# Kernel optimization log

Measured on AMD Instinct MI355X. Metric: run time of the kernel, lower is better.

## Reference

```python
import jax, jax.numpy as jnp
import numpy as np

D = 512
H = 8
HD = D // H
EPS = 1e-5
NEG_INF = -1e30


def _ln(x, g, b):
    mu = jnp.mean(x, axis=-1, keepdims=True)
    var = jnp.mean(jnp.square(x - mu), axis=-1, keepdims=True)
    return (x - mu) * jax.lax.rsqrt(var + EPS) * g + b


def setup_inputs() -> dict:
    key = jax.random.key(0)
    ks = jax.random.split(key, 8)
    V, M, S = 128, 128, 514  # seq includes 2 head tokens (cls+dist)
    inp = {
        "video_embeds": jax.random.normal(ks[0], (V, D), jnp.float32),
        "music_features": jax.random.normal(ks[1], (M, S, D), jnp.float32),
        "music_masks": jnp.ones((M, S - 2), jnp.int32),
    }
    wk = jax.random.split(ks[2], 5)
    for name, k in zip(["Wq", "Wk", "Wv", "Wo", "Wl"], wk):
        inp[name] = jax.random.normal(k, (D, D), jnp.float32) * 0.02
    for name in ["bq", "bk", "bv", "bo", "bl"]:
        inp[name] = jnp.zeros((D,), jnp.float32)
    for name in ["g1", "g2", "g3"]:
        inp[name] = jnp.ones((D,), jnp.float32)
    for name in ["b1", "b2", "b3"]:
        inp[name] = jnp.zeros((D,), jnp.float32)
    return inp


def reference(video_embeds, music_features, music_masks,
              Wq, bq, Wk, bk, Wv, bv, Wo, bo, Wl, bl,
              g1, b1, g2, b2, g3, b3):
    # drop cls + dist tokens
    mf = music_features[:, 2:, :]  # (M, f, D)
    ve = _ln(video_embeds, g1, b1)  # (V, D)
    mf = _ln(mf, g1, b1)
    V = ve.shape[0]
    M, f, _ = mf.shape

    q = (ve @ Wq.T + bq).reshape(V, H, HD).transpose(1, 0, 2)        # (H, V, hd)
    k = (mf @ Wk.T + bk).reshape(M, f, H, HD).transpose(0, 2, 1, 3)  # (M, H, f, hd)
    v = (mf @ Wv.T + bv).reshape(M, f, H, HD).transpose(0, 2, 1, 3)  # (M, H, f, hd)

    logits = jnp.einsum('hvd,mhfd->vmhf', q, k) / np.sqrt(HD).astype(np.float32)
    mask = music_masks[None, :, None, :]  # (1, M, 1, f)
    logits = jnp.where(mask == 0, NEG_INF, logits)
    w = jax.nn.softmax(logits, axis=-1)
    attn = jnp.einsum('vmhf,mhfd->vmhd', w, v).reshape(V, M, D)
    attn = attn @ Wo.T + bo

    attn = _ln(attn, g2, b2)
    out = attn + (attn @ Wl.T + bl)  # dropout = identity in eval
    return _ln(out, g3, b3)
```

## Files before the change

### kernel.cpp

```cpp
#include <hip/hip_runtime.h>
#include <hip/hip_bf16.h>

typedef unsigned int uint;
typedef unsigned short ushort;
typedef __bf16 bf16;
typedef bf16 bf16x8 __attribute__((ext_vector_type(8)));
typedef float f32x4 __attribute__((ext_vector_type(4)));
typedef ushort ushort4v __attribute__((ext_vector_type(4)));

__device__ __forceinline__ float bf2f(ushort u) {
  union { uint u; float f; } v; v.u = ((uint)u) << 16; return v.f;
}
__device__ __forceinline__ ushort f2bf(float f) {
  union { float f; uint u; } v; v.f = f;
  uint u = v.u;
  uint r = (u + 0x7fffu + ((u >> 16) & 1u)) >> 16;
  return (ushort)r;
}

__device__ __forceinline__ void gl2lds16(const void* g, void* l) {
  __builtin_amdgcn_global_load_lds(
      (const __attribute__((address_space(1))) void*)g,
      (__attribute__((address_space(3))) void*)l, 16, 0, 0);
}

__device__ __forceinline__ void ln_rows0(
    int nrows, int blk, int nblk, int tid,
    const float* __restrict__ srcA,
    const float* __restrict__ g, const float* __restrict__ b,
    ushort* __restrict__ dst)
{
  const int l = tid & 63;
  const int nw = nblk * 4;
  for (int row = blk * 4 + (tid >> 6); row < nrows; row += nw) {
    const float* s = srcA + (size_t)row * 512;
    float x[8];
    float4 a0 = *(const float4*)(s + l * 4);
    float4 a1 = *(const float4*)(s + 256 + l * 4);
    x[0] = a0.x; x[1] = a0.y; x[2] = a0.z; x[3] = a0.w;
    x[4] = a1.x; x[5] = a1.y; x[6] = a1.z; x[7] = a1.w;
    float sum = 0.f, sq = 0.f;
    #pragma unroll
    for (int j = 0; j < 8; ++j) { sum += x[j]; sq += x[j] * x[j]; }
    #pragma unroll
    for (int o = 1; o < 64; o <<= 1) {
      sum += __shfl_xor(sum, o);
      sq  += __shfl_xor(sq, o);
    }
    float mu = sum * (1.f / 512.f);
    float var = sq * (1.f / 512.f) - mu * mu;
    float rstd = rsqrtf(var + 1e-5f);
    float4 g0 = *(const float4*)(g + l * 4);
    float4 g1 = *(const float4*)(g + 256 + l * 4);
    float4 b0 = *(const float4*)(b + l * 4);
    float4 b1 = *(const float4*)(b + 256 + l * 4);
    float gv[8] = {g0.x,g0.y,g0.z,g0.w,g1.x,g1.y,g1.z,g1.w};
    float bv[8] = {b0.x,b0.y,b0.z,b0.w,b1.x,b1.y,b1.z,b1.w};
    ushort* d = dst + (size_t)row * 512;
    ushort4v p0, p1;
    #pragma unroll
    for (int j = 0; j < 4; ++j) {
      p0[j] = f2bf((x[j] - mu) * rstd * gv[j] + bv[j]);
      p1[j] = f2bf((x[4+j] - mu) * rstd * gv[4+j] + bv[4+j]);
    }
    *(ushort4v*)(d + l * 4) = p0;
    *(ushort4v*)(d + 256 + l * 4) = p1;
  }
}

__device__ __forceinline__ void ln_pair(
    int mode, int wid, int tid,
    const void* __restrict__ srcA, const void* __restrict__ srcB,
    const float* __restrict__ g, const float* __restrict__ b,
    void* __restrict__ dst)
{
  const int l = tid & 63;
  const int r0 = wid * 2, r1 = r0 + 1;
  float x0[8], x1[8];
  if (mode == 1) {
    int mm0 = r0 >> 9, fi0 = r0 & 511;
    int mm1 = r1 >> 9, fi1 = r1 & 511;
    const float* s0 = (const float*)srcA + ((size_t)mm0 * 514 + 2 + fi0) * 512;
    const float* s1 = (const float*)srcA + ((size_t)mm1 * 514 + 2 + fi1) * 512;
    float4 a0 = *(const float4*)(s0 + l * 4);
    float4 a1 = *(const float4*)(s0 + 256 + l * 4);
    float4 c0 = *(const float4*)(s1 + l * 4);
    float4 c1 = *(const float4*)(s1 + 256 + l * 4);
    x0[0]=a0.x; x0[1]=a0.y; x0[2]=a0.z; x0[3]=a0.w;
    x0[4]=a1.x; x0[5]=a1.y; x0[6]=a1.z; x0[7]=a1.w;
    x1[0]=c0.x; x1[1]=c0.y; x1[2]=c0.z; x1[3]=c0.w;
    x1[4]=c1.x; x1[5]=c1.y; x1[6]=c1.z; x1[7]=c1.w;
  } else if (mode == 2) {
    const ushort* s0 = (const ushort*)srcA + (size_t)r0 * 512;
    const ushort* s1 = (const ushort*)srcA + (size_t)r1 * 512;
    uint4 u0 = *(const uint4*)(s0 + l * 8);
    uint4 u1 = *(const uint4*)(s1 + l * 8);
    x0[0]=bf2f((ushort)u0.x); x0[1]=bf2f((ushort)(u0.x>>16));
    x0[2]=bf2f((ushort)u0.y); x0[3]=bf2f((ushort)(u0.y>>16));
    x0[4]=bf2f((ushort)u0.z); x0[5]=bf2f((ushort)(u0.z>>16));
    x0[6]=bf2f((ushort)u0.w); x0[7]=bf2f((ushort)(u0.w>>16));
    x1[0]=bf2f((ushort)u1.x); x1[1]=bf2f((ushort)(u1.x>>16));
    x1[2]=bf2f((ushort)u1.y); x1[3]=bf2f((ushort)(u1.y>>16));
    x1[4]=bf2f((ushort)u1.z); x1[5]=bf2f((ushort)(u1.z>>16));
    x1[6]=bf2f((ushort)u1.w); x1[7]=bf2f((ushort)(u1.w>>16));
  } else {
    const ushort* sa0 = (const ushort*)srcA + (size_t)r0 * 512;
    const ushort* sb0 = (const ushort*)srcB + (size_t)r0 * 512;
    const ushort* sa1 = (const ushort*)srcA + (size_t)r1 * 512;
    const ushort* sb1 = (const ushort*)srcB + (size_t)r1 * 512;
    uint4 ua0 = *(const uint4*)(sa0 + l * 8);
    uint4 ub0 = *(const uint4*)(sb0 + l * 8);
    uint4 ua1 = *(const uint4*)(sa1 + l * 8);
    uint4 ub1 = *(const uint4*)(sb1 + l * 8);
    x0[0]=bf2f((ushort)ua0.x)+bf2f((ushort)ub0.x);
    x0[1]=bf2f((ushort)(ua0.x>>16))+bf2f((ushort)(ub0.x>>16));
    x0[2]=bf2f((ushort)ua0.y)+bf2f((ushort)ub0.y);
    x0[3]=bf2f((ushort)(ua0.y>>16))+bf2f((ushort)(ub0.y>>16));
    x0[4]=bf2f((ushort)ua0.z)+bf2f((ushort)ub0.z);
    x0[5]=bf2f((ushort)(ua0.z>>16))+bf2f((ushort)(ub0.z>>16));
    x0[6]=bf2f((ushort)ua0.w)+bf2f((ushort)ub0.w);
    x0[7]=bf2f((ushort)(ua0.w>>16))+bf2f((ushort)(ub0.w>>16));
    x1[0]=bf2f((ushort)ua1.x)+bf2f((ushort)ub1.x);
    x1[1]=bf2f((ushort)(ua1.x>>16))+bf2f((ushort)(ub1.x>>16));
    x1[2]=bf2f((ushort)ua1.y)+bf2f((ushort)ub1.y);
    x1[3]=bf2f((ushort)(ua1.y>>16))+bf2f((ushort)(ub1.y>>16));
    x1[4]=bf2f((ushort)ua1.z)+bf2f((ushort)ub1.z);
    x1[5]=bf2f((ushort)(ua1.z>>16))+bf2f((ushort)(ub1.z>>16));
    x1[6]=bf2f((ushort)ua1.w)+bf2f((ushort)ub1.w);
    x1[7]=bf2f((ushort)(ua1.w>>16))+bf2f((ushort)(ub1.w>>16));
  }
  float s0 = 0.f, q0 = 0.f, s1 = 0.f, q1 = 0.f;
  #pragma unroll
  for (int j = 0; j < 8; ++j) {
    s0 += x0[j]; q0 += x0[j] * x0[j];
    s1 += x1[j]; q1 += x1[j] * x1[j];
  }
  #pragma unroll
  for (int o = 1; o < 64; o <<= 1) {
    s0 += __shfl_xor(s0, o); q0 += __shfl_xor(q0, o);
    s1 += __shfl_xor(s1, o); q1 += __shfl_xor(q1, o);
  }
  float mu0 = s0 * (1.f/512.f), mu1 = s1 * (1.f/512.f);
  float rstd0 = rsqrtf(q0 * (1.f/512.f) - mu0 * mu0 + 1e-5f);
  float rstd1 = rsqrtf(q1 * (1.f/512.f) - mu1 * mu1 + 1e-5f);

  float gv[8], bv[8];
  if (mode == 1) {
    float4 g0 = *(const float4*)(g + l * 4);
    float4 g1v = *(const float4*)(g + 256 + l * 4);
    float4 b0 = *(const float4*)(b + l * 4);
    float4 b1v = *(const float4*)(b + 256 + l * 4);
    gv[0]=g0.x; gv[1]=g0.y; gv[2]=g0.z; gv[3]=g0.w;
    gv[4]=g1v.x; gv[5]=g1v.y; gv[6]=g1v.z; gv[7]=g1v.w;
    bv[0]=b0.x; bv[1]=b0.y; bv[2]=b0.z; bv[3]=b0.w;
    bv[4]=b1v.x; bv[5]=b1v.y; bv[6]=b1v.z; bv[7]=b1v.w;
  } else {
    float4 g0 = *(const float4*)(g + l * 8);
    float4 g1v = *(const float4*)(g + l * 8 + 4);
    float4 b0 = *(const float4*)(b + l * 8);
    float4 b1v = *(const float4*)(b + l * 8 + 4);
    gv[0]=g0.x; gv[1]=g0.y; gv[2]=g0.z; gv[3]=g0.w;
    gv[4]=g1v.x; gv[5]=g1v.y; gv[6]=g1v.z; gv[7]=g1v.w;
    bv[0]=b0.x; bv[1]=b0.y; bv[2]=b0.z; bv[3]=b0.w;
    bv[4]=b1v.x; bv[5]=b1v.y; bv[6]=b1v.z; bv[7]=b1v.w;
  }
  if (mode == 1) {
    ushort* d0 = (ushort*)dst + (size_t)r0 * 512;
    ushort* d1 = (ushort*)dst + (size_t)r1 * 512;
    ushort4v p00, p01, p10, p11;
    #pragma unroll
    for (int j = 0; j < 4; ++j) {
      p00[j] = f2bf((x0[j]-mu0)*rstd0*gv[j]+bv[j]);
      p01[j] = f2bf((x0[4+j]-mu0)*rstd0*gv[4+j]+bv[4+j]);
      p10[j] = f2bf((x1[j]-mu1)*rstd1*gv[j]+bv[j]);
      p11[j] = f2bf((x1[4+j]-mu1)*rstd1*gv[4+j]+bv[4+j]);
    }
    *(ushort4v*)(d0 + l * 4) = p00;
    *(ushort4v*)(d0 + 256 + l * 4) = p01;
    *(ushort4v*)(d1 + l * 4) = p10;
    *(ushort4v*)(d1 + 256 + l * 4) = p11;
  } else if (mode == 2) {
    ushort* d0 = (ushort*)dst + (size_t)r0 * 512;
    ushort* d1 = (ushort*)dst + (size_t)r1 * 512;
    uint4 o0, o1;
    float y;
    uint t;
    y = (x0[0]-mu0)*rstd0*gv[0]+bv[0]; t = f2bf(y);
    o0.x = t | ((uint)f2bf((x0[1]-mu0)*rstd0*gv[1]+bv[1]) << 16);
    o0.y = (uint)f2bf((x0[2]-mu0)*rstd0*gv[2]+bv[2]) | ((uint)f2bf((x0[3]-mu0)*rstd0*gv[3]+bv[3]) << 16);
    o0.z = (uint)f2bf((x0[4]-mu0)*rstd0*gv[4]+bv[4]) | ((uint)f2bf((x0[5]-mu0)*rstd0*gv[5]+bv[5]) << 16);
    o0.w = (uint)f2bf((x0[6]-mu0)*rstd0*gv[6]+bv[6]) | ((uint)f2bf((x0[7]-mu0)*rstd0*gv[7]+bv[7]) << 16);
    o1.x = (uint)f2bf((x1[0]-mu1)*rstd1*gv[0]+bv[0]) | ((uint)f2bf((x1[1]-mu1)*rstd1*gv[1]+bv[1]) << 16);
    o1.y = (uint)f2bf((x1[2]-mu1)*rstd1*gv[2]+bv[2]) | ((uint)f2bf((x1[3]-mu1)*rstd1*gv[3]+bv[3]) << 16);
    o1.z = (uint)f2bf((x1[4]-mu1)*rstd1*gv[4]+bv[4]) | ((uint)f2bf((x1[5]-mu1)*rstd1*gv[5]+bv[5]) << 16);
    o1.w = (uint)f2bf((x1[6]-mu1)*rstd1*gv[6]+bv[6]) | ((uint)f2bf((x1[7]-mu1)*rstd1*gv[7]+bv[7]) << 16);
    *(uint4*)(d0 + l * 8) = o0;
    *(uint4*)(d1 + l * 8) = o1;
  } else {
    float* d0 = (float*)dst + (size_t)r0 * 512;
    float* d1 = (float*)dst + (size_t)r1 * 512;
    float4 a0, a1, c0, c1;
    a0.x=(x0[0]-mu0)*rstd0*gv[0]+bv[0]; a0.y=(x0[1]-mu0)*rstd0*gv[1]+bv[1];
    a0.z=(x0[2]-mu0)*rstd0*gv[2]+bv[2]; a0.w=(x0[3]-mu0)*rstd0*gv[3]+bv[3];
    a1.x=(x0[4]-mu0)*rstd0*gv[4]+bv[4]; a1.y=(x0[5]-mu0)*rstd0*gv[5]+bv[5];
    a1.z=(x0[6]-mu0)*rstd0*gv[6]+bv[6]; a1.w=(x0[7]-mu0)*rstd0*gv[7]+bv[7];
    c0.x=(x1[0]-mu1)*rstd1*gv[0]+bv[0]; c0.y=(x1[1]-mu1)*rstd1*gv[1]+bv[1];
    c0.z=(x1[2]-mu1)*rstd1*gv[2]+bv[2]; c0.w=(x1[3]-mu1)*rstd1*gv[3]+bv[3];
    c1.x=(x1[4]-mu1)*rstd1*gv[4]+bv[4]; c1.y=(x1[5]-mu1)*rstd1*gv[5]+bv[5];
    c1.z=(x1[6]-mu1)*rstd1*gv[6]+bv[6]; c1.w=(x1[7]-mu1)*rstd1*gv[7]+bv[7];
    *(float4*)(d0 + l * 8) = a0;
    *(float4*)(d0 + l * 8 + 4) = a1;
    *(float4*)(d1 + l * 8) = c0;
    *(float4*)(d1 + l * 8 + 4) = c1;
  }
}

__global__ __launch_bounds__(256) void ln512p(
    int mode, const void* __restrict__ srcA, const void* __restrict__ srcB,
    const float* __restrict__ g, const float* __restrict__ b,
    void* __restrict__ dst)
{
  ln_pair(mode, blockIdx.x * 4 + (threadIdx.x >> 6), threadIdx.x, srcA, srcB, g, b, dst);
}

struct PreArgs {
  const float* s0; const float* s1; const float* s2; const float* s3; const float* s4;
  ushort* d0; ushort* d1; ushort* d2; ushort* d3; ushort* d4;
  const float* video; const float* music;
  const float* g1; const float* b1;
  ushort* veln; ushort* mfln;
};
__global__ __launch_bounds__(256) void preamble(PreArgs a) {
  int bb = blockIdx.x;
  if (bb < 640) {
    int t = bb * 256 + threadIdx.x;
    int which = t >> 15;
    int e = (t & 32767) * 8;
    const float* s = which == 0 ? a.s0 : which == 1 ? a.s1 : which == 2 ? a.s2 : which == 3 ? a.s3 : a.s4;
    ushort*      d = which == 0 ? a.d0 : which == 1 ? a.d1 : which == 2 ? a.d2 : which == 3 ? a.d3 : a.d4;
    float4 v0 = *(const float4*)(s + e);
    float4 v1 = *(const float4*)(s + e + 4);
    uint4 o;
    o.x = (uint)f2bf(v0.x) | ((uint)f2bf(v0.y) << 16);
    o.y = (uint)f2bf(v0.z) | ((uint)f2bf(v0.w) << 16);
    o.z = (uint)f2bf(v1.x) | ((uint)f2bf(v1.y) << 16);
    o.w = (uint)f2bf(v1.z) | ((uint)f2bf(v1.w) << 16);
    *(uint4*)(d + e) = o;
  } else if (bb < 672) {
    ln_rows0(128, bb - 640, 32, threadIdx.x, a.video, a.g1, a.b1, a.veln);
  } else {
    ln_pair(1, (bb - 672) * 4 + (threadIdx.x >> 6), threadIdx.x,
            a.music, nullptr, a.g1, a.b1, a.mfln);
  }
}

__global__ __launch_bounds__(256) void gemm_t3(
    const ushort* __restrict__ A, const ushort* __restrict__ W,
    const float* __restrict__ bias, ushort* __restrict__ C,
    float scale, int vt_mode,
    const ushort* __restrict__ Aq, const ushort* __restrict__ Wqp,
    const float* __restrict__ bqp, ushort* __restrict__ Qout, int qy)
{
  __shared__ __align__(16) ushort As[2][128 * 64];
  __shared__ __align__(16) ushort Bs[2][128 * 64];
  const int tid = threadIdx.x;
  const int w = tid >> 6, l = tid & 63;
  const int lg = l >> 4, lr = l & 15;
  const int wr = w >> 1, wc = w & 1;

  int row0, col0;
  const bool isq = ((int)blockIdx.y == qy);
  if (isq) {
    A = Aq; W = Wqp; bias = bqp; C = Qout; scale = 0.125f; vt_mode = 0;
    row0 = 0; col0 = blockIdx.x * 128;
  } else {
    int nwg = gridDim.x * (qy >= 0 ? qy : gridDim.y);
    int bid = blockIdx.y * gridDim.x + blockIdx.x;
    if ((nwg & 7) == 0) bid = (bid & 7) * (nwg >> 3) + (bid >> 3);
    row0 = (bid / gridDim.x) * 128;
    col0 = (bid % gridDim.x) * 128;
  }

  f32x4 acc[4][4];
  #pragma unroll
  for (int i = 0; i < 4; i++)
    #pragma unroll
    for (int j = 0; j < 4; j++) { f32x4 z = {0.f,0.f,0.f,0.f}; acc[i][j] = z; }

  size_t asrc[4], wsrc[4]; int ldst[4];
  #pragma unroll
  for (int c2 = 0; c2 < 4; ++c2) {
    int c = c2 * 256 + tid;
    int r = c >> 3, j = c & 7;
    int koff = (j ^ (r & 7)) * 8;
    asrc[c2] = (size_t)(row0 + r) * 512 + koff;
    wsrc[c2] = (size_t)(col0 + r) * 512 + koff;
    ldst[c2] = (c2 * 256 + w * 64) * 8;
  }

  auto stage = [&](int pb, int kk) {
    #pragma unroll
    for (int c2 = 0; c2 < 4; ++c2) {
      gl2lds16(A + asrc[c2] + kk * 64, &As[pb][ldst[c2]]);
      gl2lds16(W + wsrc[c2] + kk * 64, &Bs[pb][ldst[c2]]);
    }
  };
  auto compute = [&](int pb) {
    #pragma unroll
    for (int ks = 0; ks < 2; ++ks) {
      bf16x8 af[4], bfr[4];
      #pragma unroll
      for (int mi = 0; mi < 4; ++mi) {
        int r = wr * 64 + mi * 16 + lr;
        af[mi] = *(const bf16x8*)(&As[pb][r * 64 + ((ks * 32 + lg * 8) ^ ((r & 7) * 8))]);
      }
      #pragma unroll
      for (int ni = 0; ni < 4; ++ni) {
        int r = wc * 64 + ni * 16 + lr;
        bfr[ni] = *(const bf16x8*)(&Bs[pb][r * 64 + ((ks * 32 + lg * 8) ^ ((r & 7) * 8))]);
      }
      #pragma unroll
      for (int mi = 0; mi < 4; ++mi)
        #pragma unroll
        for (int ni = 0; ni < 4; ++ni)
          acc[mi][ni] = __builtin_amdgcn_mfma_f32_16x16x32_bf16(af[mi], bfr[ni], acc[mi][ni], 0, 0, 0);
    }
  };

  stage(0, 0);
  __syncthreads();
  int cur = 0;
  #pragma unroll
  for (int kk = 0; kk < 7; ++kk) {
    stage(cur ^ 1, kk + 1);
    compute(cur);
    __syncthreads();
    cur ^= 1;
  }
  compute(cur);
  __syncthreads();

  ushort* img = (ushort*)As;
  #pragma unroll
  for (int ni = 0; ni < 4; ++ni) {
    float bc = bias[col0 + wc * 64 + ni * 16 + lr];
    #pragma unroll
    for (int mi = 0; mi < 4; ++mi) {
      #pragma unroll
      for (int e = 0; e < 4; ++e) {
        float v = (acc[mi][ni][e] + bc) * scale;
        int x, y;
        if (!vt_mode) { x = wr * 64 + mi * 16 + lg * 4 + e; y = wc * 64 + ni * 16 + lr; }
        else          { x = wc * 64 + ni * 16 + lr;         y = wr * 64 + mi * 16 + lg * 4 + e; }
        int byte = x * 256 + ((y * 2) ^ (((x >> 2) & 3) * 32));
        img[byte >> 1] = f2bf(v);
      }
    }
  }
  __syncthreads();
  {
    const int m = row0 >> 9, fi0 = row0 & 511;
    #pragma unroll
    for (int pass = 0; pass < 8; ++pass) {
      int r = pass * 16 + (tid >> 4);
      int cb = tid & 15;
      int byte = r * 256 + ((cb * 16) ^ (((r >> 2) & 3) * 32));
      uint4 d = *(const uint4*)(img + (byte >> 1));
      if (!vt_mode)
        *(uint4*)(C + (size_t)(row0 + r) * 512 + col0 + cb * 8) = d;
      else
        *(uint4*)(C + (size_t)(m * 512 + col0 + r) * 512 + fi0 + cb * 8) = d;
    }
  }
}

__global__ __launch_bounds__(256) void attn_kernel(
    const ushort* __restrict__ q, const ushort* __restrict__ k,
    const ushort* __restrict__ vt, const int* __restrict__ masks,
    ushort* __restrict__ attn)
{
  __shared__ __align__(16) ushort Qs[128 * 64];
  __shared__ __align__(16) ushort Ks[64 * 64];
  __shared__ __align__(16) ushort Vs[64 * 64];
  __shared__ __align__(16) ushort Ps[4][32 * 64];
  __shared__ float maskf[64];
  __shared__ float stats[4][32];

  const int tid = threadIdx.x;
  const int w = tid >> 6, l = tid & 63;
  const int lg = l >> 4, lr = l & 15;
  const int m = blockIdx.x >> 3, h = blockIdx.x & 7;

  const size_t kbase = (size_t)(m * 512) * 512 + h * 64;
  const size_t vbase = (size_t)(m * 512 + h * 64) * 512;

  #pragma unroll
  for (int c2 = 0; c2 < 4; ++c2) {
    int c = c2 * 256 + tid;
    int r = c >> 3, j = c & 7;
    gl2lds16(q + (size_t)r * 512 + h * 64 + ((j * 8) ^ ((r & 7) * 8)),
             Qs + (c2 * 256 + w * 64) * 8);
  }

  f32x4 acc[2][4];
  #pragma unroll
  for (int i = 0; i < 2; i++)
    #pragma unroll
    for (int j = 0; j < 4; j++) { f32x4 z = {0.f,0.f,0.f,0.f}; acc[i][j] = z; }
  float m_run[2] = {-INFINITY, -INFINITY};
  float l_run[2] = {0.f, 0.f};
  bf16x8 qf[2][2];

  for (int it = 0; it < 8; ++it) {
    const int f0 = it * 64;
    #pragma unroll
    for (int c2 = 0; c2 < 2; ++c2) {
      int c = c2 * 256 + tid;
      int r = c >> 3, j = c & 7;
      int off = (j * 8) ^ ((r & 7) * 8);
      gl2lds16(k + kbase + (size_t)(f0 + r) * 512 + off, Ks + (c2 * 256 + w * 64) * 8);
      gl2lds16(vt + vbase + (size_t)r * 512 + f0 + off, Vs + (c2 * 256 + w * 64) * 8);
    }
    if (tid < 64) maskf[tid] = masks[m * 512 + f0 + tid] ? 0.f : -1e30f;
    __syncthreads();

    if (it == 0) {
      #pragma unroll
      for (int nv = 0; nv < 2; ++nv)
        #pragma unroll
        for (int k2 = 0; k2 < 2; ++k2) {
          int v = w * 32 + nv * 16 + lr;
          qf[nv][k2] = *(const bf16x8*)(Qs + v * 64 + ((k2 * 32 + lg * 8) ^ ((v & 7) * 8)));
        }
    }

    f32x4 s[4][2];
    #pragma unroll
    for (int mi = 0; mi < 4; mi++)
      #pragma unroll
      for (int nv = 0; nv < 2; nv++) { f32x4 z = {0.f,0.f,0.f,0.f}; s[mi][nv] = z; }
    #pragma unroll
    for (int k2 = 0; k2 < 2; ++k2) {
      bf16x8 kf[4];
      #pragma unroll
      for (int mi = 0; mi < 4; ++mi) {
        int f = mi * 16 + lr;
        kf[mi] = *(const bf16x8*)(Ks + f * 64 + ((k2 * 32 + lg * 8) ^ ((f & 7) * 8)));
      }
      __builtin_amdgcn_s_setprio(1);
      #pragma unroll
      for (int mi = 0; mi < 4; ++mi)
        #pragma unroll
        for (int nv = 0; nv < 2; ++nv)
          s[mi][nv] = __builtin_amdgcn_mfma_f32_16x16x32_bf16(kf[mi], qf[nv][k2], s[mi][nv], 0, 0, 0);
      __builtin_amdgcn_s_setprio(0);
    }

    float mk[4][4];
    #pragma unroll
    for (int mi = 0; mi < 4; mi++)
      #pragma unroll
      for (int e = 0; e < 4; e++) mk[mi][e] = maskf[mi * 16 + lg * 4 + e];

    #pragma unroll
    for (int nv = 0; nv < 2; ++nv) {
      float cmax = -INFINITY;
      #pragma unroll
      for (int mi = 0; mi < 4; mi++)
        #pragma unroll
        for (int e = 0; e < 4; e++) {
          s[mi][nv][e] += mk[mi][e];
          cmax = fmaxf(cmax, s[mi][nv][e]);
        }
      cmax = fmaxf(cmax, __shfl_xor(cmax, 16));
      cmax = fmaxf(cmax, __shfl_xor(cmax, 32));
      float mnew = fmaxf(m_run[nv], cmax);
      float sc = __expf(m_run[nv] - mnew);
      float csum = 0.f;
      int vloc = nv * 16 + lr;
      #pragma unroll
      for (int mi = 0; mi < 4; mi++) {
        ushort4v pk;
        #pragma unroll
        for (int e = 0; e < 4; e++) {
          float p = __expf(s[mi][nv][e] - mnew);
          csum += p;
          pk[e] = f2bf(p);
        }
        int f = mi * 16 + lg * 4;
        *(ushort4v*)(&Ps[w][vloc * 64 + (f ^ ((vloc & 7) * 8))]) = pk;
      }
      csum += __shfl_xor(csum, 16);
      csum += __shfl_xor(csum, 32);
      l_run[nv] = l_run[nv] * sc + csum;
      m_run[nv] = mnew;
      if (lg == 0) stats[w][vloc] = sc;
    }

    #pragma unroll
    for (int mi2 = 0; mi2 < 2; ++mi2)
      #pragma unroll
      for (int e = 0; e < 4; ++e) {
        float sc = stats[w][mi2 * 16 + lg * 4 + e];
        #pragma unroll
        for (int nd = 0; nd < 4; ++nd) acc[mi2][nd][e] *= sc;
      }

    #pragma unroll
    for (int k2 = 0; k2 < 2; ++k2) {
      bf16x8 pf[2], vf[4];
      #pragma unroll
      for (int mi2 = 0; mi2 < 2; ++mi2) {
        int vloc = mi2 * 16 + lr;
        pf[mi2] = *(const bf16x8*)(&Ps[w][vloc * 64 + ((k2 * 32 + lg * 8) ^ ((vloc & 7) * 8))]);
      }
      #pragma unroll
      for (int nd = 0; nd < 4; ++nd) {
        int d = nd * 16 + lr;
        vf[nd] = *(const bf16x8*)(Vs + d * 64 + ((k2 * 32 + lg * 8) ^ ((d & 7) * 8)));
      }
      __builtin_amdgcn_s_setprio(1);
      #pragma unroll
      for (int mi2 = 0; mi2 < 2; ++mi2)
        #pragma unroll
        for (int nd = 0; nd < 4; ++nd)
          acc[mi2][nd] = __builtin_amdgcn_mfma_f32_16x16x32_bf16(pf[mi2], vf[nd], acc[mi2][nd], 0, 0, 0);
      __builtin_amdgcn_s_setprio(0);
    }
    __syncthreads();
  }

  #pragma unroll
  for (int nv = 0; nv < 2; ++nv)
    if (lg == 0) stats[w][nv * 16 + lr] = 1.f / l_run[nv];
  #pragma unroll
  for (int mi2 = 0; mi2 < 2; ++mi2)
    #pragma unroll
    for (int e = 0; e < 4; ++e) {
      float invl = stats[w][mi2 * 16 + lg * 4 + e];
      int vg = w * 32 + mi2 * 16 + lg * 4 + e;
      #pragma unroll
      for (int nd = 0; nd < 4; ++nd) {
        int d = nd * 16 + lr;
        attn[(size_t)(vg * 128 + m) * 512 + h * 64 + d] = f2bf(acc[mi2][nd][e] * invl);
      }
    }
}

extern "C" void kernel_launch(void* const* d_in, const int* in_sizes, int n_in,
                              void* d_out, int out_size, void* d_ws, size_t ws_size,
                              hipStream_t stream) {
  const float* video = (const float*)d_in[0];
  const float* music = (const float*)d_in[1];
  const int*   masks = (const int*)d_in[2];
  const float* Wq = (const float*)d_in[3];
  const float* Wk = (const float*)d_in[4];
  const float* Wv = (const float*)d_in[5];
  const float* Wo = (const float*)d_in[6];
  const float* Wl = (const float*)d_in[7];
  const float* bq = (const float*)d_in[8];
  const float* bk = (const float*)d_in[9];
  const float* bv = (const float*)d_in[10];
  const float* bo = (const float*)d_in[11];
  const float* bl = (const float*)d_in[12];
  const float* g1 = (const float*)d_in[13];
  const float* g2 = (const float*)d_in[14];
  const float* g3 = (const float*)d_in[15];
  const float* b1 = (const float*)d_in[16];
  const float* b2 = (const float*)d_in[17];
  const float* b3 = (const float*)d_in[18];

  char* ws = (char*)d_ws;
  ushort* mfln = (ushort*)(ws);
  ushort* kbuf = (ushort*)(ws + 67108864);
  ushort* vtb  = (ushort*)(ws + 134217728);
  ushort* attn = (ushort*)(ws + 201326592);
  ushort* c1   = (ushort*)(ws + 218103808);
  ushort* xbuf = (ushort*)(ws + 234881024);
  ushort* veln = (ushort*)(ws + 251658240);
  ushort* qbuf = (ushort*)(ws + 251789312);
  ushort* wqb  = (ushort*)(ws + 251920384);
  ushort* wkb  = wqb + 262144;
  ushort* wvb  = wkb + 262144;
  ushort* wob  = wvb + 262144;
  ushort* wlb  = wob + 262144;

  PreArgs pa = {Wq, Wk, Wv, Wo, Wl, wqb, wkb, wvb, wob, wlb,
                video, music, g1, b1, veln, mfln};
  preamble<<<8864, 256, 0, stream>>>(pa);

  gemm_t3<<<dim3(4, 513), 256, 0, stream>>>(
      mfln, wkb, bk, kbuf, 1.f, 0, veln, wqb, bq, qbuf, 512);
  gemm_t3<<<dim3(4, 512), 256, 0, stream>>>(
      mfln, wvb, bv, vtb, 1.f, 1, nullptr, nullptr, nullptr, nullptr, -1);

  attn_kernel<<<1024, 256, 0, stream>>>(qbuf, kbuf, vtb, masks, attn);

  gemm_t3<<<dim3(4, 128), 256, 0, stream>>>(
      attn, wob, bo, c1, 1.f, 0, nullptr, nullptr, nullptr, nullptr, -1);
  ln512p<<<2048, 256, 0, stream>>>(2, c1, nullptr, g2, b2, xbuf);
  gemm_t3<<<dim3(4, 128), 256, 0, stream>>>(
      xbuf, wlb, bl, c1, 1.f, 0, nullptr, nullptr, nullptr, nullptr, -1);
  ln512p<<<2048, 256, 0, stream>>>(3, xbuf, c1, g3, b3, d_out);
}
```

Measured before the change: 328.8 us.

## Use 256-row 512-thread GEMM tiles and write epilogue directly to global

Adds a gemm_t3w kernel with 256x128 tiles and 8 waves, so each block reuses its weight tile across twice as many rows, and uses it for the K, V, Wo and Wl projections. The Q projection is split out of the K launch into its own small launch. The epilogue no longer stages results through LDS for coalesced 16-byte stores. It now writes scattered 2-byte or 8-byte stores directly to global memory, which removes a barrier and the LDS pass but risks poorly coalesced writes.

```diff
diff --git a/kernel.cpp b/kernel.cpp
--- a/kernel.cpp
+++ b/kernel.cpp
@@ -183,10 +183,7 @@
     ushort* d0 = (ushort*)dst + (size_t)r0 * 512;
     ushort* d1 = (ushort*)dst + (size_t)r1 * 512;
     uint4 o0, o1;
-    float y;
-    uint t;
-    y = (x0[0]-mu0)*rstd0*gv[0]+bv[0]; t = f2bf(y);
-    o0.x = t | ((uint)f2bf((x0[1]-mu0)*rstd0*gv[1]+bv[1]) << 16);
+    o0.x = (uint)f2bf((x0[0]-mu0)*rstd0*gv[0]+bv[0]) | ((uint)f2bf((x0[1]-mu0)*rstd0*gv[1]+bv[1]) << 16);
     o0.y = (uint)f2bf((x0[2]-mu0)*rstd0*gv[2]+bv[2]) | ((uint)f2bf((x0[3]-mu0)*rstd0*gv[3]+bv[3]) << 16);
     o0.z = (uint)f2bf((x0[4]-mu0)*rstd0*gv[4]+bv[4]) | ((uint)f2bf((x0[5]-mu0)*rstd0*gv[5]+bv[5]) << 16);
     o0.w = (uint)f2bf((x0[6]-mu0)*rstd0*gv[6]+bv[6]) | ((uint)f2bf((x0[7]-mu0)*rstd0*gv[7]+bv[7]) << 16);
@@ -257,9 +254,7 @@
 __global__ __launch_bounds__(256) void gemm_t3(
     const ushort* __restrict__ A, const ushort* __restrict__ W,
     const float* __restrict__ bias, ushort* __restrict__ C,
-    float scale, int vt_mode,
-    const ushort* __restrict__ Aq, const ushort* __restrict__ Wqp,
-    const float* __restrict__ bqp, ushort* __restrict__ Qout, int qy)
+    float scale, int vt_mode)
 {
   __shared__ __align__(16) ushort As[2][128 * 64];
   __shared__ __align__(16) ushort Bs[2][128 * 64];
@@ -268,18 +263,11 @@
   const int lg = l >> 4, lr = l & 15;
   const int wr = w >> 1, wc = w & 1;
 
-  int row0, col0;
-  const bool isq = ((int)blockIdx.y == qy);
-  if (isq) {
-    A = Aq; W = Wqp; bias = bqp; C = Qout; scale = 0.125f; vt_mode = 0;
-    row0 = 0; col0 = blockIdx.x * 128;
-  } else {
-    int nwg = gridDim.x * (qy >= 0 ? qy : gridDim.y);
-    int bid = blockIdx.y * gridDim.x + blockIdx.x;
-    if ((nwg & 7) == 0) bid = (bid & 7) * (nwg >> 3) + (bid >> 3);
-    row0 = (bid / gridDim.x) * 128;
-    col0 = (bid % gridDim.x) * 128;
-  }
+  int nwg = gridDim.x * gridDim.y;
+  int bid = blockIdx.y * gridDim.x + blockIdx.x;
+  if ((nwg & 7) == 0) bid = (bid & 7) * (nwg >> 3) + (bid >> 3);
+  const int bx = bid % gridDim.x, by = bid / gridDim.x;
+  const int row0 = by * 128, col0 = bx * 128;
 
   f32x4 acc[4][4];
   #pragma unroll
@@ -338,38 +326,133 @@
     cur ^= 1;
   }
   compute(cur);
+
+  #pragma unroll
+  for (int ni = 0; ni < 4; ++ni) {
+    int cg = col0 + wc * 64 + ni * 16 + lr;
+    float bc = bias[cg];
+    #pragma unroll
+    for (int mi = 0; mi < 4; ++mi) {
+      int rg0 = row0 + wr * 64 + mi * 16 + lg * 4;
+      if (!vt_mode) {
+        #pragma unroll
+        for (int e = 0; e < 4; ++e) {
+          float v = (acc[mi][ni][e] + bc) * scale;
+          C[(size_t)(rg0 + e) * 512 + cg] = f2bf(v);
+        }
+      } else {
+        int m = rg0 >> 9, fi = rg0 & 511;
+        ushort4v pk;
+        #pragma unroll
+        for (int e = 0; e < 4; ++e) pk[e] = f2bf((acc[mi][ni][e] + bc) * scale);
+        *(ushort4v*)(C + (size_t)(m * 512 + cg) * 512 + fi) = pk;
+      }
+    }
+  }
+}
+
+__global__ __launch_bounds__(512) void gemm_t3w(
+    const ushort* __restrict__ A, const ushort* __restrict__ W,
+    const float* __restrict__ bias, ushort* __restrict__ C,
+    float scale, int vt_mode)
+{
+  __shared__ __align__(16) ushort As[2][256 * 64];
+  __shared__ __align__(16) ushort Bs[2][128 * 64];
+  const int tid = threadIdx.x;
+  const int w = tid >> 6, l = tid & 63;
+  const int lg = l >> 4, lr = l & 15;
+  const int wr = w >> 1, wc = w & 1;
+
+  int nwg = gridDim.x * gridDim.y;
+  int bid = blockIdx.y * gridDim.x + blockIdx.x;
+  if ((nwg & 7) == 0) bid = (bid & 7) * (nwg >> 3) + (bid >> 3);
+  const int bx = bid % gridDim.x, by = bid / gridDim.x;
+  const int row0 = by * 256, col0 = bx * 128;
+
+  f32x4 acc[4][4];
+  #pragma unroll
+  for (int i = 0; i < 4; i++)
+    #pragma unroll
+    for (int j = 0; j < 4; j++) { f32x4 z = {0.f,0.f,0.f,0.f}; acc[i][j] = z; }
+
+  size_t asrc[4], wsrc[2]; int aldst[4], wldst[2];
+  {
+    int r = tid >> 3, j = tid & 7;
+    int koff = (j ^ (r & 7)) * 8;
+    #pragma unroll
+    for (int c2 = 0; c2 < 4; ++c2) {
+      asrc[c2] = (size_t)(row0 + c2 * 64 + r) * 512 + koff;
+      aldst[c2] = ((c2 * 64 + (w * 8)) * 64);
+    }
+    #pragma unroll
+    for (int c2 = 0; c2 < 2; ++c2) {
+      wsrc[c2] = (size_t)(col0 + c2 * 64 + r) * 512 + koff;
+      wldst[c2] = ((c2 * 64 + (w * 8)) * 64);
+    }
+  }
+
+  auto stage = [&](int pb, int kk) {
+    #pragma unroll
+    for (int c2 = 0; c2 < 4; ++c2)
+      gl2lds16(A + asrc[c2] + kk * 64, &As[pb][aldst[c2] + 0]);
+    #pragma unroll
+    for (int c2 = 0; c2 < 2; ++c2)
+      gl2lds16(W + wsrc[c2] + kk * 64, &Bs[pb][wldst[c2] + 0]);
+  };
+  auto compute = [&](int pb) {
+    #pragma unroll
+    for (int ks = 0; ks < 2; ++ks) {
+      bf16x8 af[4], bfr[4];
+      #pragma unroll
+      for (int mi = 0; mi < 4; ++mi) {
+        int r = wr * 64 + mi * 16 + lr;
+        af[mi] = *(const bf16x8*)(&As[pb][r * 64 + ((ks * 32 + lg * 8) ^ ((r & 7) * 8))]);
+      }
+      #pragma unroll
+      for (int ni = 0; ni < 4; ++ni) {
+        int r = wc * 64 + ni * 16 + lr;
+        bfr[ni] = *(const bf16x8*)(&Bs[pb][r * 64 + ((ks * 32 + lg * 8) ^ ((r & 7) * 8))]);
+      }
+      #pragma unroll
+      for (int mi = 0; mi < 4; ++mi)
+        #pragma unroll
+        for (int ni = 0; ni < 4; ++ni)
+          acc[mi][ni] = __builtin_amdgcn_mfma_f32_16x16x32_bf16(af[mi], bfr[ni], acc[mi][ni], 0, 0, 0);
+    }
+  };
+
+  stage(0, 0);
   __syncthreads();
-
-  ushort* img = (ushort*)As;
+  int cur = 0;
+  #pragma unroll
+  for (int kk = 0; kk < 7; ++kk) {
+    stage(cur ^ 1, kk + 1);
+    compute(cur);
+    __syncthreads();
+    cur ^= 1;
+  }
+  compute(cur);
+
   #pragma unroll
   for (int ni = 0; ni < 4; ++ni) {
-    float bc = bias[col0 + wc * 64 + ni * 16 + lr];
+    int cg = col0 + wc * 64 + ni * 16 + lr;
+    float bc = bias[cg];
     #pragma unroll
     for (int mi = 0; mi < 4; ++mi) {
-      #pragma unroll
-      for (int e = 0; e < 4; ++e) {
-        float v = (acc[mi][ni][e] + bc) * scale;
-        int x, y;
-        if (!vt_mode) { x = wr * 64 + mi * 16 + lg * 4 + e; y = wc * 64 + ni * 16 + lr; }
-        else          { x = wc * 64 + ni * 16 + lr;         y = wr * 64 + mi * 16 + lg * 4 + e; }
-        int byte = x * 256 + ((y * 2) ^ (((x >> 2) & 3) * 32));
-        img[byte >> 1] = f2bf(v);
-      }
-    }
-  }
-  __syncthreads();
-  {
-    const int m = row0 >> 9, fi0 = row0 & 511;
-    #pragma unroll
-    for (int pass = 0; pass < 8; ++pass) {
-      int r = pass * 16 + (tid >> 4);
-      int cb = tid & 15;
-      int byte = r * 256 + ((cb * 16) ^ (((r >> 2) & 3) * 32));
-      uint4 d = *(const uint4*)(img + (byte >> 1));
-      if (!vt_mode)
-        *(uint4*)(C + (size_t)(row0 + r) * 512 + col0 + cb * 8) = d;
-      else
-        *(uint4*)(C + (size_t)(m * 512 + col0 + r) * 512 + fi0 + cb * 8) = d;
+      int rg0 = row0 + wr * 64 + mi * 16 + lg * 4;
+      if (!vt_mode) {
+        #pragma unroll
+        for (int e = 0; e < 4; ++e) {
+          float v = (acc[mi][ni][e] + bc) * scale;
+          C[(size_t)(rg0 + e) * 512 + cg] = f2bf(v);
+        }
+      } else {
+        int m = rg0 >> 9, fi = rg0 & 511;
+        ushort4v pk;
+        #pragma unroll
+        for (int e = 0; e < 4; ++e) pk[e] = f2bf((acc[mi][ni][e] + bc) * scale);
+        *(ushort4v*)(C + (size_t)(m * 512 + cg) * 512 + fi) = pk;
+      }
     }
   }
 }
@@ -589,17 +672,14 @@
                 video, music, g1, b1, veln, mfln};
   preamble<<<8864, 256, 0, stream>>>(pa);
 
-  gemm_t3<<<dim3(4, 513), 256, 0, stream>>>(
-      mfln, wkb, bk, kbuf, 1.f, 0, veln, wqb, bq, qbuf, 512);
-  gemm_t3<<<dim3(4, 512), 256, 0, stream>>>(
-      mfln, wvb, bv, vtb, 1.f, 1, nullptr, nullptr, nullptr, nullptr, -1);
+  gemm_t3<<<dim3(4, 1), 256, 0, stream>>>(veln, wqb, bq, qbuf, 0.125f, 0);
+  gemm_t3w<<<dim3(4, 256), 512, 0, stream>>>(mfln, wkb, bk, kbuf, 1.f, 0);
+  gemm_t3w<<<dim3(4, 256), 512, 0, stream>>>(mfln, wvb, bv, vtb, 1.f, 1);
 
   attn_kernel<<<1024, 256, 0, stream>>>(qbuf, kbuf, vtb, masks, attn);
 
-  gemm_t3<<<dim3(4, 128), 256, 0, stream>>>(
-      attn, wob, bo, c1, 1.f, 0, nullptr, nullptr, nullptr, nullptr, -1);
+  gemm_t3w<<<dim3(4, 64), 512, 0, stream>>>(attn, wob, bo, c1, 1.f, 0);
   ln512p<<<2048, 256, 0, stream>>>(2, c1, nullptr, g2, b2, xbuf);
-  gemm_t3<<<dim3(4, 128), 256, 0, stream>>>(
-      xbuf, wlb, bl, c1, 1.f, 0, nullptr, nullptr, nullptr, nullptr, -1);
+  gemm_t3w<<<dim3(4, 64), 512, 0, stream>>>(xbuf, wlb, bl, c1, 1.f, 0);
   ln512p<<<2048, 256, 0, stream>>>(3, xbuf, c1, g3, b3, d_out);
 }
```

Measured after the change: 282.7 us. -14.0%, faster.
